# Kernel tuning notes

Measured on AMD Instinct MI355X. Metric: run time of the kernel, lower is better.

Reference implementation:

```python
import jax, jax.numpy as jnp
import numpy as np

T, N, D, H, E = 8, 50000, 128, 128, 800000


def setup_inputs() -> dict:
    key = jax.random.key(0)
    ks = jax.random.split(key, 32)
    s = 0.05
    inp = {
        "x_seq": jax.random.normal(ks[0], (T, N, D), dtype=jnp.float32),
        "edge_index_seq": jax.random.randint(ks[1], (T, 2, E), 0, N, dtype=jnp.int32),
    }
    i = 2
    def p(shape):
        nonlocal i
        w = jax.random.normal(ks[i], shape, dtype=jnp.float32) * s
        i += 1
        return w
    # layer 0 (input_dim=D)
    inp.update(W_in0=p((D, H)), b_in0=p((H,)), W_h0=p((H, H)), b_h0=p((H,)),
               Wu0=p((2 * H, H)), bu0=p((H,)), Wr0=p((2 * H, H)), br0=p((H,)),
               Wc0=p((2 * H, H)), bc0=p((H,)))
    # layer 1 (input_dim=H)
    inp.update(W_in1=p((H, H)), b_in1=p((H,)), W_h1=p((H, H)), b_h1=p((H,)),
               Wu1=p((2 * H, H)), bu1=p((H,)), Wr1=p((2 * H, H)), br1=p((H,)),
               Wc1=p((2 * H, H)), bc1=p((H,)))
    inp.update(W_out=p((H, H)), b_out=p((H,)))
    return inp


def _gcn(x, W, b, src, dst, dinv, n):
    h = x @ W
    coef = (dinv[src] * dinv[dst])[:, None]
    agg = jax.ops.segment_sum(h[src] * coef, dst, num_segments=n)
    agg = agg + h * (dinv * dinv)[:, None]  # self-loop term
    return agg + b


def _cell(x, src, dst, dinv, h_prev, W_in, b_in, W_h, b_h, Wu, bu, Wr, br, Wc, bc):
    n = x.shape[0]
    cur = jax.nn.relu(_gcn(x, W_in, b_in, src, dst, dinv, n))
    cur = _gcn(cur, W_h, b_h, src, dst, dinv, n)
    comb = jnp.concatenate([cur, h_prev], axis=1)
    u = jax.nn.sigmoid(comb @ Wu + bu)
    r = jax.nn.sigmoid(comb @ Wr + br)
    cand = jnp.tanh(jnp.concatenate([cur, r * h_prev], axis=1) @ Wc + bc)
    return (1.0 - u) * h_prev + u * cand


def reference(x_seq, edge_index_seq,
              W_in0, b_in0, W_h0, b_h0, Wu0, bu0, Wr0, br0, Wc0, bc0,
              W_in1, b_in1, W_h1, b_h1, Wu1, bu1, Wr1, br1, Wc1, bc1,
              W_out, b_out):
    n = x_seq.shape[1]

    def step(carry, xs):
        h0, h1 = carry
        x_t, ei_t = xs
        src, dst = ei_t[0], ei_t[1]
        deg = jax.ops.segment_sum(jnp.ones(ei_t.shape[1], x_t.dtype), dst, num_segments=n) + 1.0
        dinv = jax.lax.rsqrt(deg)
        h0 = _cell(x_t, src, dst, dinv, h0, W_in0, b_in0, W_h0, b_h0, Wu0, bu0, Wr0, br0, Wc0, bc0)
        h1 = _cell(h0, src, dst, dinv, h1, W_in1, b_in1, W_h1, b_h1, Wu1, bu1, Wr1, br1, Wc1, bc1)
        emb = h1 @ W_out + b_out
        return (h0, h1), emb

    h0 = jnp.zeros((n, W_h0.shape[0]), x_seq.dtype)
    h1 = jnp.zeros((n, W_h1.shape[0]), x_seq.dtype)
    _, embs = jax.lax.scan(step, (h0, h1), (x_seq, edge_index_seq))
    return embs  # [T, N, H]
```

## Files before the change

### kernel.cpp

```cpp
#include <hip/hip_runtime.h>
#include <math.h>

#define TT 8
#define NN 50000
#define HH 128
#define EE 800000

#define M_SCALE 0
#define M_GATE  1
#define M_CAND  2
#define M_OUT   3

typedef __attribute__((ext_vector_type(8))) short short8;
typedef __attribute__((ext_vector_type(4))) float f32x4;

__device__ __forceinline__ float sigmoidf_(float x){ return 1.0f/(1.0f+__expf(-x)); }

__device__ __forceinline__ short f2bf(float f){
  unsigned u = __float_as_uint(f);
  u += 0x7fff + ((u>>16)&1);
  return (short)(u>>16);
}
__device__ __forceinline__ float bf2f(short h){
  return __uint_as_float(((unsigned)(unsigned short)h)<<16);
}


__global__ void count_kernel(const int* __restrict__ dst, int* __restrict__ counts){
  int e = blockIdx.x*256 + threadIdx.x;
  if (e < EE) atomicAdd(&counts[dst[e]], 1);
}

__global__ void scan_kernel(const int* __restrict__ counts, int* __restrict__ offs,
                            float* __restrict__ dinv){
  __shared__ int part[1024];
  const int t = threadIdx.x;
  const int per = (NN + 1023)/1024;
  int beg = t*per; int end = beg+per;
  if (end > NN) end = NN;
  if (beg > NN) beg = NN;
  int s = 0;
  for (int i=beg;i<end;i++) s += counts[i];
  part[t] = s; __syncthreads();
  for (int d=1; d<1024; d<<=1){
    int v = (t>=d) ? part[t-d] : 0;
    __syncthreads();
    part[t] += v;
    __syncthreads();
  }
  int run = part[t] - s;
  for (int i=beg;i<end;i++){
    offs[i] = run;
    int c = counts[i];
    run += c;
    dinv[i] = rsqrtf((float)c + 1.0f);
  }
  if (t==1023) offs[NN] = run;
}

__global__ void fill_kernel(const int* __restrict__ src, const int* __restrict__ dst,
                            const int* __restrict__ offs, int* __restrict__ cursor,
                            int* __restrict__ csr){
  int e = blockIdx.x*256 + threadIdx.x;
  if (e < EE){
    int d = dst[e];
    int p = atomicAdd(&cursor[d], 1);
    csr[offs[d]+p] = src[e];
  }
}


__global__ void split_kernel(const float* __restrict__ W, short* __restrict__ WT_hi,
                             short* __restrict__ WT_lo, int K){
  int idx = blockIdx.x*256 + threadIdx.x;
  if (idx >= K*128) return;
  int c = idx & 127, k = idx >> 7;
  float v = W[k*128 + c];
  short h = f2bf(v);
  short l = f2bf(v - bf2f(h));
  WT_hi[(size_t)c*K + k] = h;
  WT_lo[(size_t)c*K + k] = l;
}

template<int RELU>
__global__ __launch_bounds__(256) void agg_kernel(
    const float* __restrict__ Ys, const int* __restrict__ csr,
    const int* __restrict__ offs, const float* __restrict__ dinv,
    const float* __restrict__ bias, float* __restrict__ out)
{
  const int node = blockIdx.x*8 + (threadIdx.x>>5);
  if (node >= NN) return;
  const int lane = threadIdx.x & 31;
  const float4* Y4 = (const float4*)Ys;
  float4 a = Y4[(size_t)node*32 + lane];
  float acc0=a.x, acc1=a.y, acc2=a.z, acc3=a.w;
  const int b = offs[node], e = offs[node+1];
  for (int j=b;j<e;j++){
    int s = csr[j];
    float4 v = Y4[(size_t)s*32 + lane];
    acc0+=v.x; acc1+=v.y; acc2+=v.z; acc3+=v.w;
  }
  const float d = dinv[node];
  const float4 bb = *(const float4*)(bias + lane*4);
  float o0 = acc0*d + bb.x;
  float o1 = acc1*d + bb.y;
  float o2 = acc2*d + bb.z;
  float o3 = acc3*d + bb.w;
  if (RELU){ o0=fmaxf(o0,0.f); o1=fmaxf(o1,0.f); o2=fmaxf(o2,0.f); o3=fmaxf(o3,0.f); }
  *(float4*)(out + (size_t)node*HH + lane*4) = make_float4(o0,o1,o2,o3);
}

template<int MODE, int K>
__global__ __launch_bounds__(256,2) void mm_mfma(
    const float* __restrict__ A1, const float* __restrict__ A2,
    const float* __restrict__ Rg,
    const short* __restrict__ WT_hi, const short* __restrict__ WT_lo,
    const float* __restrict__ bias, const float* __restrict__ dinv,
    const float* __restrict__ U, float* __restrict__ out)
{
  __shared__ __align__(16) short Ah[128*64];
  __shared__ __align__(16) short Al[128*64];
  __shared__ __align__(16) short Bh[128*64];
  __shared__ __align__(16) short Bl[128*64];

  const int tid  = threadIdx.x;
  const int lane = tid & 63;
  const int w    = tid >> 6;
  const int bm0  = blockIdx.x * 128;
  const int row_w = (w>>1)*64, col_w = (w&1)*64;
  const int l15 = lane & 15, l4 = lane >> 4;

  f32x4 acc[4][4];
  #pragma unroll
  for (int mt=0;mt<4;mt++)
    #pragma unroll
    for (int nt=0;nt<4;nt++) acc[mt][nt] = (f32x4)(0.0f);

  const int srow  = tid >> 1;
  const int shalf = (tid & 1) * 32;
  const int grow  = bm0 + srow;
  const unsigned skey = (unsigned)(srow & 7) << 4;

  for (int kc = 0; kc < K/64; ++kc){
    const bool fromA2 = (K==256) && (kc >= 2);
    const float* asrc = fromA2 ? A2 : A1;
    const int koff = fromA2 ? (kc-2)*64 : kc*64;
    float av[32];
    if (grow < NN){
      const float* ap = asrc + (size_t)grow*HH + koff + shalf;
      #pragma unroll
      for (int j=0;j<8;j++) *(float4*)&av[j*4] = *(const float4*)(ap + j*4);
      if constexpr (MODE==M_CAND){
        if (fromA2){
          const float* rp = Rg + (size_t)grow*HH + koff + shalf;
          #pragma unroll
          for (int j=0;j<8;j++){
            float4 rv = *(const float4*)(rp + j*4);
            av[j*4+0]*=rv.x; av[j*4+1]*=rv.y; av[j*4+2]*=rv.z; av[j*4+3]*=rv.w;
          }
        }
      }
    } else {
      #pragma unroll
      for (int j=0;j<32;j++) av[j] = 0.f;
    }
    #pragma unroll
    for (int g=0; g<4; g++){
      short8 vh, vl;
      #pragma unroll
      for (int e=0;e<8;e++){
        float f = av[g*8+e];
        short h = f2bf(f);
        vh[e] = h;
        vl[e] = f2bf(f - bf2f(h));
      }
      unsigned byte = ((unsigned)(shalf*2 + g*16)) ^ skey;
      int idx = srow*64 + (int)(byte>>1);
      *(short8*)&Ah[idx] = vh;
      *(short8*)&Al[idx] = vl;
    }
    {
      const short* sh = WT_hi + (size_t)srow*K + kc*64 + shalf;
      const short* sl = WT_lo + (size_t)srow*K + kc*64 + shalf;
      #pragma unroll
      for (int g=0; g<4; g++){
        short8 vh = *(const short8*)(sh + g*8);
        short8 vl = *(const short8*)(sl + g*8);
        unsigned byte = ((unsigned)(shalf*2 + g*16)) ^ skey;
        int idx = srow*64 + (int)(byte>>1);
        *(short8*)&Bh[idx] = vh;
        *(short8*)&Bl[idx] = vl;
      }
    }
    __syncthreads();
    #pragma unroll
    for (int kk=0; kk<2; kk++){
      short8 ahf[4], alf[4], bhf[4], blf[4];
      #pragma unroll
      for (int mt=0; mt<4; mt++){
        int r = row_w + mt*16 + l15;
        unsigned byte = ((unsigned)(kk*64 + l4*16)) ^ ((unsigned)(r&7)<<4);
        int idx = r*64 + (int)(byte>>1);
        ahf[mt] = *(const short8*)&Ah[idx];
        alf[mt] = *(const short8*)&Al[idx];
      }
      #pragma unroll
      for (int nt=0; nt<4; nt++){
        int c = col_w + nt*16 + l15;
        unsigned byte = ((unsigned)(kk*64 + l4*16)) ^ ((unsigned)(c&7)<<4);
        int idx = c*64 + (int)(byte>>1);
        bhf[nt] = *(const short8*)&Bh[idx];
        blf[nt] = *(const short8*)&Bl[idx];
      }
      #pragma unroll
      for (int mt=0; mt<4; mt++)
        #pragma unroll
        for (int nt=0; nt<4; nt++){
          acc[mt][nt] = __builtin_amdgcn_mfma_f32_16x16x32_bf16(ahf[mt], bhf[nt], acc[mt][nt], 0,0,0);
          acc[mt][nt] = __builtin_amdgcn_mfma_f32_16x16x32_bf16(ahf[mt], blf[nt], acc[mt][nt], 0,0,0);
          acc[mt][nt] = __builtin_amdgcn_mfma_f32_16x16x32_bf16(alf[mt], bhf[nt], acc[mt][nt], 0,0,0);
        }
    }
    __syncthreads();
  }

  float bs[4] = {0.f,0.f,0.f,0.f};
  if constexpr (MODE != M_SCALE){
    #pragma unroll
    for (int nt=0;nt<4;nt++) bs[nt] = bias[col_w + nt*16 + l15];
  }
  #pragma unroll
  for (int mt=0; mt<4; mt++){
    #pragma unroll
    for (int r=0; r<4; r++){
      int row = bm0 + row_w + mt*16 + l4*4 + r;
      if (row < NN){
        float dv = 0.f;
        if constexpr (MODE==M_SCALE) dv = dinv[row];
        #pragma unroll
        for (int nt=0; nt<4; nt++){
          int col = col_w + nt*16 + l15;
          float v = acc[mt][nt][r];
          if constexpr (MODE==M_SCALE){
            v *= dv;
          } else if constexpr (MODE==M_GATE){
            v = sigmoidf_(v + bs[nt]);
          } else if constexpr (MODE==M_CAND){
            size_t ix = (size_t)row*HH + col;
            float u = U[ix], hp = A2[ix];
            v = (1.f-u)*hp + u*tanhf(v + bs[nt]);
          } else {
            v += bs[nt];
          }
          out[(size_t)row*HH + col] = v;
        }
      }
    }
  }
}


extern "C" void kernel_launch(void* const* d_in, const int* in_sizes, int n_in,
                              void* d_out, int out_size, void* d_ws, size_t ws_size,
                              hipStream_t stream)
{
  const float* x_seq = (const float*)d_in[0];
  const int*   eidx  = (const int*)  d_in[1];
  const float* W_in0=(const float*)d_in[2];
  const float* b_in0=(const float*)d_in[3];
  const float* W_h0 =(const float*)d_in[4];
  const float* b_h0 =(const float*)d_in[5];
  const float* Wu0  =(const float*)d_in[6];
  const float* bu0  =(const float*)d_in[7];
  const float* Wr0  =(const float*)d_in[8];
  const float* br0  =(const float*)d_in[9];
  const float* Wc0  =(const float*)d_in[10];
  const float* bc0  =(const float*)d_in[11];
  const float* W_in1=(const float*)d_in[12];
  const float* b_in1=(const float*)d_in[13];
  const float* W_h1 =(const float*)d_in[14];
  const float* b_h1 =(const float*)d_in[15];
  const float* Wu1  =(const float*)d_in[16];
  const float* bu1  =(const float*)d_in[17];
  const float* Wr1  =(const float*)d_in[18];
  const float* br1  =(const float*)d_in[19];
  const float* Wc1  =(const float*)d_in[20];
  const float* bc1  =(const float*)d_in[21];
  const float* W_out=(const float*)d_in[22];
  const float* b_out=(const float*)d_in[23];
  float* out = (float*)d_out;

  char* p = (char*)d_ws;
  auto take = [&](size_t bytes)->void*{
    void* r = (void*)p;
    p += ((bytes + 255) & ~((size_t)255));
    return r;
  };
  const size_t fmat = (size_t)NN*HH*sizeof(float);
  float* h0   = (float*)take(fmat);
  float* h1   = (float*)take(fmat);
  float* T1   = (float*)take(fmat);
  float* T2   = (float*)take(fmat);
  float* Rb   = (float*)take(fmat);
  int*   counts=(int*)take((size_t)NN*4);
  int*   cursor=(int*)take((size_t)NN*4);
  int*   offs  =(int*)take((size_t)(NN+1)*4);
  int*   csr   =(int*)take((size_t)EE*4);
  float* dinv  =(float*)take((size_t)NN*4);

  const float* Wsrc[11] = {W_in0, W_h0, Wu0, Wr0, Wc0, W_in1, W_h1, Wu1, Wr1, Wc1, W_out};
  const int    Wk[11]   = {128,   128,  256, 256, 256, 128,   128,  256, 256, 256, 128};
  short* Wh[11]; short* Wl[11];
  for (int i=0;i<11;i++){
    Wh[i] = (short*)take((size_t)Wk[i]*128*2);
    Wl[i] = (short*)take((size_t)Wk[i]*128*2);
  }

  hipMemsetAsync(h0, 0, fmat, stream);
  hipMemsetAsync(h1, 0, fmat, stream);

  for (int i=0;i<11;i++)
    split_kernel<<<(Wk[i]*128+255)/256, 256, 0, stream>>>(Wsrc[i], Wh[i], Wl[i], Wk[i]);

  dim3 mmG((NN+127)/128), mmB(256);
  dim3 agG((NN+7)/8), agB(256);
  dim3 eG((EE+255)/256), eB(256);

  for (int t=0; t<TT; ++t){
    const int* src = eidx + (size_t)t*2*EE;
    const int* dst = src + EE;
    const float* xt = x_seq + (size_t)t*NN*HH;
    float* outt = out + (size_t)t*NN*HH;

    hipMemsetAsync(counts, 0, (size_t)NN*4, stream);
    hipMemsetAsync(cursor, 0, (size_t)NN*4, stream);
    count_kernel<<<eG,eB,0,stream>>>(dst, counts);
    scan_kernel<<<1,1024,0,stream>>>(counts, offs, dinv);
    fill_kernel<<<eG,eB,0,stream>>>(src, dst, offs, cursor, csr);

    mm_mfma<M_SCALE,128><<<mmG,mmB,0,stream>>>(xt, nullptr, nullptr, Wh[0],Wl[0], nullptr, dinv, nullptr, T1);
    agg_kernel<1><<<agG,agB,0,stream>>>(T1, csr, offs, dinv, b_in0, T2);
    mm_mfma<M_SCALE,128><<<mmG,mmB,0,stream>>>(T2, nullptr, nullptr, Wh[1],Wl[1], nullptr, dinv, nullptr, T1);
    agg_kernel<0><<<agG,agB,0,stream>>>(T1, csr, offs, dinv, b_h0, T2);
    mm_mfma<M_GATE,256><<<mmG,mmB,0,stream>>>(T2, h0, nullptr, Wh[2],Wl[2], bu0, nullptr, nullptr, T1);
    mm_mfma<M_GATE,256><<<mmG,mmB,0,stream>>>(T2, h0, nullptr, Wh[3],Wl[3], br0, nullptr, nullptr, Rb);
    mm_mfma<M_CAND,256><<<mmG,mmB,0,stream>>>(T2, h0, Rb, Wh[4],Wl[4], bc0, nullptr, T1, h0);

    mm_mfma<M_SCALE,128><<<mmG,mmB,0,stream>>>(h0, nullptr, nullptr, Wh[5],Wl[5], nullptr, dinv, nullptr, T1);
    agg_kernel<1><<<agG,agB,0,stream>>>(T1, csr, offs, dinv, b_in1, T2);
    mm_mfma<M_SCALE,128><<<mmG,mmB,0,stream>>>(T2, nullptr, nullptr, Wh[6],Wl[6], nullptr, dinv, nullptr, T1);
    agg_kernel<0><<<agG,agB,0,stream>>>(T1, csr, offs, dinv, b_h1, T2);
    mm_mfma<M_GATE,256><<<mmG,mmB,0,stream>>>(T2, h1, nullptr, Wh[7],Wl[7], bu1, nullptr, nullptr, T1);
    mm_mfma<M_GATE,256><<<mmG,mmB,0,stream>>>(T2, h1, nullptr, Wh[8],Wl[8], br1, nullptr, nullptr, Rb);
    mm_mfma<M_CAND,256><<<mmG,mmB,0,stream>>>(T2, h1, Rb, Wh[9],Wl[9], bc1, nullptr, T1, h1);

    mm_mfma<M_OUT,128><<<mmG,mmB,0,stream>>>(h1, nullptr, nullptr, Wh[10],Wl[10], b_out, nullptr, nullptr, outt);
  }
}
```

Before: 6.033 ms.

## Store intermediates as pre-split bf16 hi/lo pairs and merge update/reset GEMMs

Intermediate activations (hidden states, GCN outputs, gate results) are stored as bf16 hi/lo pairs, so the MFMA GEMMs load them directly instead of re-splitting fp32 in every tile, and the aggregation kernel gathers 2x2-byte pairs in place of fp32. The update and reset gate GEMMs are fused into one launch with a 2-wide grid over a concatenated weight matrix, and the reset gate is multiplied by h_prev in the epilogue, so the candidate GEMM reads r*h already formed. This cuts launches, removes the per-tile split work and drops the separate multiply in the candidate loader. Total bytes moved stay about the same, while the hi/lo representation adds some rounding error.

```diff
diff --git a/kernel.cpp b/kernel.cpp
--- a/kernel.cpp
+++ b/kernel.cpp
@@ -7,11 +7,12 @@
 #define EE 800000
 
 #define M_SCALE 0
-#define M_GATE  1
+#define M_UR    1
 #define M_CAND  2
 #define M_OUT   3
 
 typedef __attribute__((ext_vector_type(8))) short short8;
+typedef __attribute__((ext_vector_type(4))) short s16x4;
 typedef __attribute__((ext_vector_type(4))) float f32x4;
 
 __device__ __forceinline__ float sigmoidf_(float x){ return 1.0f/(1.0f+__expf(-x)); }
@@ -23,6 +24,9 @@
 }
 __device__ __forceinline__ float bf2f(short h){
   return __uint_as_float(((unsigned)(unsigned short)h)<<16);
+}
+__device__ __forceinline__ void split2(float f, short& h, short& l){
+  h = f2bf(f); l = f2bf(f - bf2f(h));
 }
 
 
@@ -69,36 +73,53 @@
   }
 }
 
-
-__global__ void split_kernel(const float* __restrict__ W, short* __restrict__ WT_hi,
-                             short* __restrict__ WT_lo, int K){
+__global__ void split_kernel(const float* __restrict__ W, short* __restrict__ WTh,
+                             short* __restrict__ WTl, int K){
   int idx = blockIdx.x*256 + threadIdx.x;
   if (idx >= K*128) return;
   int c = idx & 127, k = idx >> 7;
-  float v = W[k*128 + c];
-  short h = f2bf(v);
-  short l = f2bf(v - bf2f(h));
-  WT_hi[(size_t)c*K + k] = h;
-  WT_lo[(size_t)c*K + k] = l;
+  short h,l; split2(W[k*128 + c], h, l);
+  WTh[(size_t)c*K + k] = h;
+  WTl[(size_t)c*K + k] = l;
+}
+__global__ void split2_kernel(const float* __restrict__ Wa, const float* __restrict__ Wb,
+                              short* __restrict__ WTh, short* __restrict__ WTl){
+  int idx = blockIdx.x*256 + threadIdx.x;
+  if (idx >= 256*256) return;
+  int c = idx & 255, k = idx >> 8;
+  const float* W = (c<128)? Wa : Wb;
+  short h,l; split2(W[k*128 + (c&127)], h, l);
+  WTh[(size_t)c*256 + k] = h;
+  WTl[(size_t)c*256 + k] = l;
 }
 
 template<int RELU>
 __global__ __launch_bounds__(256) void agg_kernel(
-    const float* __restrict__ Ys, const int* __restrict__ csr,
-    const int* __restrict__ offs, const float* __restrict__ dinv,
-    const float* __restrict__ bias, float* __restrict__ out)
+    const short* __restrict__ Yh, const short* __restrict__ Yl,
+    const int* __restrict__ csr, const int* __restrict__ offs,
+    const float* __restrict__ dinv, const float* __restrict__ bias,
+    short* __restrict__ Oh, short* __restrict__ Ol)
 {
   const int node = blockIdx.x*8 + (threadIdx.x>>5);
   if (node >= NN) return;
   const int lane = threadIdx.x & 31;
-  const float4* Y4 = (const float4*)Ys;
-  float4 a = Y4[(size_t)node*32 + lane];
-  float acc0=a.x, acc1=a.y, acc2=a.z, acc3=a.w;
+  const s16x4* Yh4 = (const s16x4*)Yh;
+  const s16x4* Yl4 = (const s16x4*)Yl;
+  s16x4 sh = Yh4[(size_t)node*32 + lane];
+  s16x4 sl = Yl4[(size_t)node*32 + lane];
+  float acc0 = bf2f(sh[0])+bf2f(sl[0]);
+  float acc1 = bf2f(sh[1])+bf2f(sl[1]);
+  float acc2 = bf2f(sh[2])+bf2f(sl[2]);
+  float acc3 = bf2f(sh[3])+bf2f(sl[3]);
   const int b = offs[node], e = offs[node+1];
   for (int j=b;j<e;j++){
     int s = csr[j];
-    float4 v = Y4[(size_t)s*32 + lane];
-    acc0+=v.x; acc1+=v.y; acc2+=v.z; acc3+=v.w;
+    s16x4 vh = Yh4[(size_t)s*32 + lane];
+    s16x4 vl = Yl4[(size_t)s*32 + lane];
+    acc0 += bf2f(vh[0])+bf2f(vl[0]);
+    acc1 += bf2f(vh[1])+bf2f(vl[1]);
+    acc2 += bf2f(vh[2])+bf2f(vl[2]);
+    acc3 += bf2f(vh[3])+bf2f(vl[3]);
   }
   const float d = dinv[node];
   const float4 bb = *(const float4*)(bias + lane*4);
@@ -107,16 +128,28 @@
   float o2 = acc2*d + bb.z;
   float o3 = acc3*d + bb.w;
   if (RELU){ o0=fmaxf(o0,0.f); o1=fmaxf(o1,0.f); o2=fmaxf(o2,0.f); o3=fmaxf(o3,0.f); }
-  *(float4*)(out + (size_t)node*HH + lane*4) = make_float4(o0,o1,o2,o3);
-}
-
-template<int MODE, int K>
+  s16x4 oh, ol; short th, tl;
+  split2(o0,th,tl); oh[0]=th; ol[0]=tl;
+  split2(o1,th,tl); oh[1]=th; ol[1]=tl;
+  split2(o2,th,tl); oh[2]=th; ol[2]=tl;
+  split2(o3,th,tl); oh[3]=th; ol[3]=tl;
+  ((s16x4*)Oh)[(size_t)node*32 + lane] = oh;
+  ((s16x4*)Ol)[(size_t)node*32 + lane] = ol;
+}
+
+template<int MODE, int K, bool A1F32>
 __global__ __launch_bounds__(256,2) void mm_mfma(
-    const float* __restrict__ A1, const float* __restrict__ A2,
-    const float* __restrict__ Rg,
-    const short* __restrict__ WT_hi, const short* __restrict__ WT_lo,
-    const float* __restrict__ bias, const float* __restrict__ dinv,
-    const float* __restrict__ U, float* __restrict__ out)
+    const float* __restrict__ A1f,
+    const short* __restrict__ A1h, const short* __restrict__ A1l,
+    const short* __restrict__ A2h, const short* __restrict__ A2l,
+    const short* __restrict__ WTh, const short* __restrict__ WTl,
+    const float* __restrict__ b0, const float* __restrict__ b1,
+    const float* __restrict__ dinv,
+    const short* __restrict__ Ph, const short* __restrict__ Pl,
+    const short* __restrict__ Qh, const short* __restrict__ Ql,
+    float* __restrict__ outf,
+    short* __restrict__ Oh, short* __restrict__ Ol,
+    short* __restrict__ O2h, short* __restrict__ O2l)
 {
   __shared__ __align__(16) short Ah[128*64];
   __shared__ __align__(16) short Al[128*64];
@@ -143,53 +176,51 @@
 
   for (int kc = 0; kc < K/64; ++kc){
     const bool fromA2 = (K==256) && (kc >= 2);
-    const float* asrc = fromA2 ? A2 : A1;
-    const int koff = fromA2 ? (kc-2)*64 : kc*64;
-    float av[32];
+    const int koff = (fromA2 ? (kc-2)*64 : kc*64) + shalf;
+    short8 vh[4], vl[4];
     if (grow < NN){
-      const float* ap = asrc + (size_t)grow*HH + koff + shalf;
-      #pragma unroll
-      for (int j=0;j<8;j++) *(float4*)&av[j*4] = *(const float4*)(ap + j*4);
-      if constexpr (MODE==M_CAND){
-        if (fromA2){
-          const float* rp = Rg + (size_t)grow*HH + koff + shalf;
+      if (A1F32 && !fromA2){
+        const float* ap = A1f + (size_t)grow*HH + koff;
+        #pragma unroll
+        for (int g=0; g<4; g++){
           #pragma unroll
-          for (int j=0;j<8;j++){
-            float4 rv = *(const float4*)(rp + j*4);
-            av[j*4+0]*=rv.x; av[j*4+1]*=rv.y; av[j*4+2]*=rv.z; av[j*4+3]*=rv.w;
+          for (int e=0;e<8;e++){
+            short h,l; split2(ap[g*8+e], h, l);
+            vh[g][e]=h; vl[g][e]=l;
           }
+        }
+      } else {
+        const short* sh = (fromA2 ? A2h : A1h) + (size_t)grow*HH + koff;
+        const short* sl = (fromA2 ? A2l : A1l) + (size_t)grow*HH + koff;
+        #pragma unroll
+        for (int g=0; g<4; g++){
+          vh[g] = *(const short8*)(sh + g*8);
+          vl[g] = *(const short8*)(sl + g*8);
         }
       }
     } else {
       #pragma unroll
-      for (int j=0;j<32;j++) av[j] = 0.f;
+      for (int g=0; g<4; g++){ vh[g] = (short8)0; vl[g] = (short8)0; }
     }
     #pragma unroll
     for (int g=0; g<4; g++){
-      short8 vh, vl;
-      #pragma unroll
-      for (int e=0;e<8;e++){
-        float f = av[g*8+e];
-        short h = f2bf(f);
-        vh[e] = h;
-        vl[e] = f2bf(f - bf2f(h));
-      }
       unsigned byte = ((unsigned)(shalf*2 + g*16)) ^ skey;
       int idx = srow*64 + (int)(byte>>1);
-      *(short8*)&Ah[idx] = vh;
-      *(short8*)&Al[idx] = vl;
+      *(short8*)&Ah[idx] = vh[g];
+      *(short8*)&Al[idx] = vl[g];
     }
     {
-      const short* sh = WT_hi + (size_t)srow*K + kc*64 + shalf;
-      const short* sl = WT_lo + (size_t)srow*K + kc*64 + shalf;
+      const int bcol = (MODE==M_UR) ? (int)(blockIdx.y*128 + srow) : srow;
+      const short* sh = WTh + (size_t)bcol*K + kc*64 + shalf;
+      const short* sl = WTl + (size_t)bcol*K + kc*64 + shalf;
       #pragma unroll
       for (int g=0; g<4; g++){
-        short8 vh = *(const short8*)(sh + g*8);
-        short8 vl = *(const short8*)(sl + g*8);
+        short8 wh = *(const short8*)(sh + g*8);
+        short8 wl = *(const short8*)(sl + g*8);
         unsigned byte = ((unsigned)(shalf*2 + g*16)) ^ skey;
         int idx = srow*64 + (int)(byte>>1);
-        *(short8*)&Bh[idx] = vh;
-        *(short8*)&Bl[idx] = vl;
+        *(short8*)&Bh[idx] = wh;
+        *(short8*)&Bl[idx] = wl;
       }
     }
     __syncthreads();
@@ -224,10 +255,12 @@
     __syncthreads();
   }
 
+  const int y = (MODE==M_UR) ? (int)blockIdx.y : 0;
   float bs[4] = {0.f,0.f,0.f,0.f};
   if constexpr (MODE != M_SCALE){
+    const float* bb = (MODE==M_UR && y==1) ? b1 : b0;
     #pragma unroll
-    for (int nt=0;nt<4;nt++) bs[nt] = bias[col_w + nt*16 + l15];
+    for (int nt=0;nt<4;nt++) bs[nt] = bb[col_w + nt*16 + l15];
   }
   #pragma unroll
   for (int mt=0; mt<4; mt++){
@@ -240,19 +273,32 @@
         #pragma unroll
         for (int nt=0; nt<4; nt++){
           int col = col_w + nt*16 + l15;
+          size_t ix = (size_t)row*HH + col;
           float v = acc[mt][nt][r];
           if constexpr (MODE==M_SCALE){
             v *= dv;
-          } else if constexpr (MODE==M_GATE){
+            short h,l; split2(v,h,l);
+            Oh[ix]=h; Ol[ix]=l;
+          } else if constexpr (MODE==M_UR){
             v = sigmoidf_(v + bs[nt]);
+            if (y==1){
+              float hp = bf2f(Qh[ix]) + bf2f(Ql[ix]);
+              v *= hp;
+              short h,l; split2(v,h,l);
+              O2h[ix]=h; O2l[ix]=l;
+            } else {
+              short h,l; split2(v,h,l);
+              Oh[ix]=h; Ol[ix]=l;
+            }
           } else if constexpr (MODE==M_CAND){
-            size_t ix = (size_t)row*HH + col;
-            float u = U[ix], hp = A2[ix];
+            float u  = bf2f(Ph[ix]) + bf2f(Pl[ix]);
+            float hp = bf2f(Qh[ix]) + bf2f(Ql[ix]);
             v = (1.f-u)*hp + u*tanhf(v + bs[nt]);
+            short h,l; split2(v,h,l);
+            Oh[ix]=h; Ol[ix]=l;
           } else {
-            v += bs[nt];
+            outf[ix] = v + bs[nt];
           }
-          out[(size_t)row*HH + col] = v;
         }
       }
     }
@@ -296,35 +342,52 @@
     p += ((bytes + 255) & ~((size_t)255));
     return r;
   };
-  const size_t fmat = (size_t)NN*HH*sizeof(float);
-  float* h0   = (float*)take(fmat);
-  float* h1   = (float*)take(fmat);
-  float* T1   = (float*)take(fmat);
-  float* T2   = (float*)take(fmat);
-  float* Rb   = (float*)take(fmat);
+  const size_t pmat = (size_t)NN*HH*sizeof(short);
+  short* h0h=(short*)take(pmat); short* h0l=(short*)take(pmat);
+  short* h1h=(short*)take(pmat); short* h1l=(short*)take(pmat);
+  short* T1h=(short*)take(pmat); short* T1l=(short*)take(pmat);
+  short* T2h=(short*)take(pmat); short* T2l=(short*)take(pmat);
+  short* RHh=(short*)take(pmat); short* RHl=(short*)take(pmat);
   int*   counts=(int*)take((size_t)NN*4);
   int*   cursor=(int*)take((size_t)NN*4);
   int*   offs  =(int*)take((size_t)(NN+1)*4);
   int*   csr   =(int*)take((size_t)EE*4);
   float* dinv  =(float*)take((size_t)NN*4);
 
-  const float* Wsrc[11] = {W_in0, W_h0, Wu0, Wr0, Wc0, W_in1, W_h1, Wu1, Wr1, Wc1, W_out};
-  const int    Wk[11]   = {128,   128,  256, 256, 256, 128,   128,  256, 256, 256, 128};
-  short* Wh[11]; short* Wl[11];
-  for (int i=0;i<11;i++){
-    Wh[i] = (short*)take((size_t)Wk[i]*128*2);
-    Wl[i] = (short*)take((size_t)Wk[i]*128*2);
-  }
-
-  hipMemsetAsync(h0, 0, fmat, stream);
-  hipMemsetAsync(h1, 0, fmat, stream);
-
-  for (int i=0;i<11;i++)
-    split_kernel<<<(Wk[i]*128+255)/256, 256, 0, stream>>>(Wsrc[i], Wh[i], Wl[i], Wk[i]);
+  short *WIh[2], *WIl[2], *WHh[2], *WHl[2], *WUh[2], *WUl[2], *WCh[2], *WCl[2];
+  for (int i=0;i<2;i++){
+    WIh[i]=(short*)take(128*128*2); WIl[i]=(short*)take(128*128*2);
+    WHh[i]=(short*)take(128*128*2); WHl[i]=(short*)take(128*128*2);
+    WUh[i]=(short*)take(256*256*2); WUl[i]=(short*)take(256*256*2);
+    WCh[i]=(short*)take(128*256*2); WCl[i]=(short*)take(128*256*2);
+  }
+  short* WOh=(short*)take(128*128*2); short* WOl=(short*)take(128*128*2);
+
+  hipMemsetAsync(h0h, 0, pmat, stream); hipMemsetAsync(h0l, 0, pmat, stream);
+  hipMemsetAsync(h1h, 0, pmat, stream); hipMemsetAsync(h1l, 0, pmat, stream);
+
+  split_kernel<<<64,256,0,stream>>>(W_in0, WIh[0], WIl[0], 128);
+  split_kernel<<<64,256,0,stream>>>(W_h0,  WHh[0], WHl[0], 128);
+  split2_kernel<<<256,256,0,stream>>>(Wu0, Wr0, WUh[0], WUl[0]);
+  split_kernel<<<128,256,0,stream>>>(Wc0,  WCh[0], WCl[0], 256);
+  split_kernel<<<64,256,0,stream>>>(W_in1, WIh[1], WIl[1], 128);
+  split_kernel<<<64,256,0,stream>>>(W_h1,  WHh[1], WHl[1], 128);
+  split2_kernel<<<256,256,0,stream>>>(Wu1, Wr1, WUh[1], WUl[1]);
+  split_kernel<<<128,256,0,stream>>>(Wc1,  WCh[1], WCl[1], 256);
+  split_kernel<<<64,256,0,stream>>>(W_out, WOh, WOl, 128);
 
   dim3 mmG((NN+127)/128), mmB(256);
+  dim3 urG((NN+127)/128, 2);
   dim3 agG((NN+7)/8), agB(256);
   dim3 eG((EE+255)/256), eB(256);
+
+  const float* bI[2] = {b_in0, b_in1};
+  const float* bH[2] = {b_h0, b_h1};
+  const float* bU[2] = {bu0, bu1};
+  const float* bR[2] = {br0, br1};
+  const float* bC[2] = {bc0, bc1};
+  short* Sh[2] = {h0h, h1h};
+  short* Sl[2] = {h0l, h1l};
 
   for (int t=0; t<TT; ++t){
     const int* src = eidx + (size_t)t*2*EE;
@@ -338,22 +401,30 @@
     scan_kernel<<<1,1024,0,stream>>>(counts, offs, dinv);
     fill_kernel<<<eG,eB,0,stream>>>(src, dst, offs, cursor, csr);
 
-    mm_mfma<M_SCALE,128><<<mmG,mmB,0,stream>>>(xt, nullptr, nullptr, Wh[0],Wl[0], nullptr, dinv, nullptr, T1);
-    agg_kernel<1><<<agG,agB,0,stream>>>(T1, csr, offs, dinv, b_in0, T2);
-    mm_mfma<M_SCALE,128><<<mmG,mmB,0,stream>>>(T2, nullptr, nullptr, Wh[1],Wl[1], nullptr, dinv, nullptr, T1);
-    agg_kernel<0><<<agG,agB,0,stream>>>(T1, csr, offs, dinv, b_h0, T2);
-    mm_mfma<M_GATE,256><<<mmG,mmB,0,stream>>>(T2, h0, nullptr, Wh[2],Wl[2], bu0, nullptr, nullptr, T1);
-    mm_mfma<M_GATE,256><<<mmG,mmB,0,stream>>>(T2, h0, nullptr, Wh[3],Wl[3], br0, nullptr, nullptr, Rb);
-    mm_mfma<M_CAND,256><<<mmG,mmB,0,stream>>>(T2, h0, Rb, Wh[4],Wl[4], bc0, nullptr, T1, h0);
-
-    mm_mfma<M_SCALE,128><<<mmG,mmB,0,stream>>>(h0, nullptr, nullptr, Wh[5],Wl[5], nullptr, dinv, nullptr, T1);
-    agg_kernel<1><<<agG,agB,0,stream>>>(T1, csr, offs, dinv, b_in1, T2);
-    mm_mfma<M_SCALE,128><<<mmG,mmB,0,stream>>>(T2, nullptr, nullptr, Wh[6],Wl[6], nullptr, dinv, nullptr, T1);
-    agg_kernel<0><<<agG,agB,0,stream>>>(T1, csr, offs, dinv, b_h1, T2);
-    mm_mfma<M_GATE,256><<<mmG,mmB,0,stream>>>(T2, h1, nullptr, Wh[7],Wl[7], bu1, nullptr, nullptr, T1);
-    mm_mfma<M_GATE,256><<<mmG,mmB,0,stream>>>(T2, h1, nullptr, Wh[8],Wl[8], br1, nullptr, nullptr, Rb);
-    mm_mfma<M_CAND,256><<<mmG,mmB,0,stream>>>(T2, h1, Rb, Wh[9],Wl[9], bc1, nullptr, T1, h1);
-
-    mm_mfma<M_OUT,128><<<mmG,mmB,0,stream>>>(h1, nullptr, nullptr, Wh[10],Wl[10], b_out, nullptr, nullptr, outt);
-  }
-}
+    for (int l=0; l<2; ++l){
+      short* hh = Sh[l]; short* hl = Sl[l];
+      if (l==0)
+        mm_mfma<M_SCALE,128,true><<<mmG,mmB,0,stream>>>(xt, nullptr,nullptr, nullptr,nullptr,
+            WIh[0],WIl[0], nullptr,nullptr, dinv, nullptr,nullptr, nullptr,nullptr,
+            nullptr, T1h,T1l, nullptr,nullptr);
+      else
+        mm_mfma<M_SCALE,128,false><<<mmG,mmB,0,stream>>>(nullptr, h0h,h0l, nullptr,nullptr,
+            WIh[1],WIl[1], nullptr,nullptr, dinv, nullptr,nullptr, nullptr,nullptr,
+            nullptr, T1h,T1l, nullptr,nullptr);
+      agg_kernel<1><<<agG,agB,0,stream>>>(T1h,T1l, csr, offs, dinv, bI[l], T2h,T2l);
+      mm_mfma<M_SCALE,128,false><<<mmG,mmB,0,stream>>>(nullptr, T2h,T2l, nullptr,nullptr,
+          WHh[l],WHl[l], nullptr,nullptr, dinv, nullptr,nullptr, nullptr,nullptr,
+          nullptr, T1h,T1l, nullptr,nullptr);
+      agg_kernel<0><<<agG,agB,0,stream>>>(T1h,T1l, csr, offs, dinv, bH[l], T2h,T2l);
+      mm_mfma<M_UR,256,false><<<urG,mmB,0,stream>>>(nullptr, T2h,T2l, hh,hl,
+          WUh[l],WUl[l], bU[l], bR[l], nullptr, nullptr,nullptr, hh,hl,
+          nullptr, T1h,T1l, RHh,RHl);
+      mm_mfma<M_CAND,256,false><<<mmG,mmB,0,stream>>>(nullptr, T2h,T2l, RHh,RHl,
+          WCh[l],WCl[l], bC[l], nullptr, nullptr, T1h,T1l, hh,hl,
+          nullptr, hh,hl, nullptr,nullptr);
+    }
+    mm_mfma<M_OUT,128,false><<<mmG,mmB,0,stream>>>(nullptr, h1h,h1l, nullptr,nullptr,
+        WOh,WOl, b_out, nullptr, nullptr, nullptr,nullptr, nullptr,nullptr,
+        outt, nullptr,nullptr, nullptr,nullptr);
+  }
+}
```

New measurement: 6.076 ms. About the same (+0.7%).
